# Performance work log

Measured on AMD Instinct MI355X. Metric: run time of the kernel, lower is better.

Reference implementation:

```python
import jax, jax.numpy as jnp
import numpy as np

NEG_INF = -1.0e9
LN_EPS = 1e-5
LEAK = 0.2


def setup_inputs() -> dict:
    key = jax.random.key(0)
    ks = jax.random.split(key, 8)
    B, C, T, N, H = 8, 64, 24, 512, 2
    hd = C // H
    x = jax.random.normal(ks[0], (B, C, T, N), dtype=jnp.float32)
    gso = jax.random.randint(ks[1], (N, N), 0, 2, dtype=jnp.int32)
    # torch nn.Linear weights are (out, in); xavier-ish scale
    s = (2.0 / (C + C)) ** 0.5
    Wq = jax.random.normal(ks[2], (C, C), dtype=jnp.float32) * s
    Wk = jax.random.normal(ks[3], (C, C), dtype=jnp.float32) * s
    Wv = jax.random.normal(ks[4], (C, C), dtype=jnp.float32) * s
    sa = (2.0 / (H + hd)) ** 0.5
    a_src = jax.random.normal(ks[5], (H, hd), dtype=jnp.float32) * sa
    a_dst = jax.random.normal(ks[6], (H, hd), dtype=jnp.float32) * sa
    ln_gamma = jnp.ones((C,), dtype=jnp.float32)
    ln_beta = jnp.zeros((C,), dtype=jnp.float32)
    return {"x": x, "gso": gso, "Wq": Wq, "Wk": Wk, "Wv": Wv,
            "a_src": a_src, "a_dst": a_dst, "ln_gamma": ln_gamma, "ln_beta": ln_beta}


def _spatial_gat(x, gso, Wq, Wk, Wv, a_src, a_dst, ln_gamma, ln_beta):
    B, C, T, N = x.shape
    H, hd = a_src.shape
    # (B, C, T, N) -> (B*T, N, C)
    xr = jnp.transpose(x, (0, 2, 3, 1)).reshape(B * T, N, C)
    # torch Linear: y = x @ W.T
    Q = jnp.einsum('bnc,dc->bnd', xr, Wq).reshape(B * T, N, H, hd)
    K = jnp.einsum('bnc,dc->bnd', xr, Wk).reshape(B * T, N, H, hd)
    V = jnp.einsum('bnc,dc->bnd', xr, Wv).reshape(B * T, N, H, hd)
    # additive GAT scores, all heads at once
    s_src = jnp.einsum('bnhd,hd->bnh', Q, a_src)  # (BT, N, H)
    s_dst = jnp.einsum('bnhd,hd->bnh', K, a_dst)  # (BT, N, H)
    scores = jax.nn.leaky_relu(s_src[:, :, None, :] + s_dst[:, None, :, :], LEAK)  # (BT, Ni, Nj, H)
    mask = jnp.where(gso == 0, jnp.float32(NEG_INF), jnp.float32(0.0))  # (N, N)
    scores = scores + mask[None, :, :, None]
    attn = jax.nn.softmax(scores, axis=2)  # softmax over destination j
    out = jnp.einsum('bijh,bjhd->bihd', attn, V)  # (BT, N, H, hd)
    out = out.reshape(B * T, N, C)
    # LayerNorm over channel dim
    mu = jnp.mean(out, axis=-1, keepdims=True)
    var = jnp.var(out, axis=-1, keepdims=True)
    out = (out - mu) * jax.lax.rsqrt(var + LN_EPS) * ln_gamma + ln_beta
    # back to (B, C, T, N)
    return jnp.transpose(out.reshape(B, T, N, C), (0, 3, 1, 2))


def reference(x, gso, Wq, Wk, Wv, a_src, a_dst, ln_gamma, ln_beta):
    return _spatial_gat(x, gso, Wq, Wk, Wv, a_src, a_dst, ln_gamma, ln_beta)
```

## Files before the change

### kernel.cpp

```cpp
#include <hip/hip_runtime.h>

#define CDIM 64
#define TDIM 24
#define NDIM 512
#define NBT  192

typedef float    float4v __attribute__((ext_vector_type(4)));
typedef _Float16 half8v  __attribute__((ext_vector_type(8)));
typedef _Float16 half4v  __attribute__((ext_vector_type(4)));
typedef _Float16 half2v  __attribute__((ext_vector_type(2)));


__device__ __forceinline__ float exp2_fast(float x) {
#if __has_builtin(__builtin_amdgcn_exp2f)
  return __builtin_amdgcn_exp2f(x);
#else
  return __expf(x * 0.69314718f);
#endif
}

struct SmemK1 {
  union {
    _Float16 xt[128][72];
    _Float16 vtb[64][136];
  } big;
  _Float16 wv[64][72];
  _Float16 wext[16][72];
};

__launch_bounds__(256, 2)
__global__ void k1_v(const float* __restrict__ x,  const float* __restrict__ Wv,
                     const float* __restrict__ Wq, const float* __restrict__ Wk,
                     const float* __restrict__ a_src, const float* __restrict__ a_dst,
                     const int* __restrict__ gso,
                     _Float16* __restrict__ VT_g,
                     float* __restrict__ s_src_g, float* __restrict__ s_dst_g,
                     unsigned char* __restrict__ maskb) {
  const int t  = threadIdx.x;
  const int bx = blockIdx.x;

  if (bx >= 768) {
    int g = (bx - 768) * 256 + t;
    const int4* gp = (const int4*)gso + (size_t)g * 4;
    unsigned w[4];
#pragma unroll
    for (int k = 0; k < 4; ++k) {
      int4 v = gp[k];
      w[k] = (v.x ? 0x000000FFu : 0u) | (v.y ? 0x0000FF00u : 0u) |
             (v.z ? 0x00FF0000u : 0u) | (v.w ? 0xFF000000u : 0u);
    }
    uint4 o; o.x = w[0]; o.y = w[1]; o.z = w[2]; o.w = w[3];
    ((uint4*)maskb)[g] = o;
    return;
  }

  __shared__ SmemK1 sm;
  const int qn = bx & 3;
  const int bt = bx >> 2;
  const int b  = bt / TDIM, tt = bt % TDIM;
  const int n0 = qn * 128;

#pragma unroll
  for (int it = 0; it < 4; ++it) {
    int idx = it * 256 + t;
    float4 vv = ((const float4*)Wv)[idx];
    int d = idx >> 4, k4 = (idx & 15) * 4;
    half4v h4; h4[0] = (_Float16)vv.x; h4[1] = (_Float16)vv.y;
    h4[2] = (_Float16)vv.z; h4[3] = (_Float16)vv.w;
    *(half4v*)&sm.wv[d][k4] = h4;
  }
  for (int z = t; z < 12 * 72; z += 256) ((_Float16*)sm.wext[4])[z] = (_Float16)0.f;
  if (t < 64) {
    int c = t;
    float s0 = 0.f, s1 = 0.f, d0 = 0.f, d1 = 0.f;
#pragma unroll
    for (int d = 0; d < 32; ++d) {
      s0 += a_src[d]      * Wq[d * 64 + c];
      s1 += a_src[32 + d] * Wq[(32 + d) * 64 + c];
      d0 += a_dst[d]      * Wk[d * 64 + c];
      d1 += a_dst[32 + d] * Wk[(32 + d) * 64 + c];
    }
    const float l2e = 1.44269504f;
    sm.wext[0][c] = (_Float16)(s0 * l2e); sm.wext[1][c] = (_Float16)(s1 * l2e);
    sm.wext[2][c] = (_Float16)(d0 * l2e); sm.wext[3][c] = (_Float16)(d1 * l2e);
  }
  for (int it = 0; it < 16; ++it) {
    int idx = it * 256 + t;
    int cp = idx >> 7, n = idx & 127;
    int c0 = cp * 2;
    const float* base = x + ((size_t)(b * CDIM + c0) * TDIM + tt) * NDIM + n0 + n;
    half2v p; p[0] = (_Float16)base[0]; p[1] = (_Float16)base[(size_t)TDIM * NDIM];
    *(half2v*)&sm.big.xt[n][c0] = p;
  }
  __syncthreads();

  const int lane = t & 63, w = t >> 6;
  const int m = lane & 15, quad = lane >> 4;
  const int mbase = w * 32;

  float4v acc[2][5];
#pragma unroll
  for (int mt = 0; mt < 2; ++mt)
#pragma unroll
    for (int nt = 0; nt < 5; ++nt)
#pragma unroll
      for (int r = 0; r < 4; ++r) acc[mt][nt][r] = 0.f;

#pragma unroll
  for (int ks = 0; ks < 2; ++ks) {
    half8v af[2], bf[5];
#pragma unroll
    for (int mt = 0; mt < 2; ++mt)
      af[mt] = *(const half8v*)&sm.big.xt[mbase + mt * 16 + m][ks * 32 + quad * 8];
#pragma unroll
    for (int nt = 0; nt < 4; ++nt)
      bf[nt] = *(const half8v*)&sm.wv[nt * 16 + m][ks * 32 + quad * 8];
    bf[4] = *(const half8v*)&sm.wext[m][ks * 32 + quad * 8];
#pragma unroll
    for (int mt = 0; mt < 2; ++mt)
#pragma unroll
      for (int nt = 0; nt < 5; ++nt)
        acc[mt][nt] = __builtin_amdgcn_mfma_f32_16x16x32_f16(af[mt], bf[nt], acc[mt][nt], 0, 0, 0);
  }

  if (m < 4) {
    float* basep = (m < 2 ? s_src_g : s_dst_g) + (size_t)(bt * 2 + (m & 1)) * NDIM;
#pragma unroll
    for (int mt = 0; mt < 2; ++mt)
#pragma unroll
      for (int r = 0; r < 4; ++r)
        basep[n0 + mbase + mt * 16 + quad * 4 + r] = acc[mt][4][r];
  }
  __syncthreads();

#pragma unroll
  for (int mt = 0; mt < 2; ++mt)
#pragma unroll
    for (int nt = 0; nt < 4; ++nt)
#pragma unroll
      for (int r = 0; r < 4; r += 2) {
        int nl = mbase + mt * 16 + quad * 4 + r;
        int c  = nt * 16 + m;
        half2v p = __builtin_bit_cast(half2v,
            __builtin_amdgcn_cvt_pkrtz(acc[mt][nt][r], acc[mt][nt][r + 1]));
        *(half2v*)&sm.big.vtb[c][nl] = p;
      }
  __syncthreads();

  const uint4* vq = (const uint4*)sm.big.vtb;
#pragma unroll
  for (int it = 0; it < 4; ++it) {
    int idx = it * 256 + t;
    int c = idx >> 4, q4 = idx & 15;
    ((uint4*)VT_g)[(size_t)(bt * 64 + c) * 64 + qn * 16 + q4] = vq[c * 17 + q4];
  }
}

struct SmemK2 {
  union {
    struct { _Float16 vt[64][128]; } s;
    struct { float otile[64][66]; float rsum[4][64]; float rsq[4][64];
             float mu[64]; float rs[64]; } e;
  } u;
  _Float16 sF16[2][512];
  _Float16 sP16[2][512];
};

__launch_bounds__(256, 4)
__global__ void k2_attn(const _Float16* __restrict__ VT_g,
                        const float* __restrict__ s_src_g, const float* __restrict__ s_dst_g,
                        const unsigned char* __restrict__ maskb,
                        const float* __restrict__ gamma, const float* __restrict__ beta,
                        float* __restrict__ out) {
  __shared__ SmemK2 sm;
  const int t     = threadIdx.x;
  const int id    = blockIdx.x;
  const int itile = (id >> 3) & 7;
  const int bt    = ((id >> 6) << 3) | (id & 7);
  const int i0    = itile * 64;
  const int b     = bt / TDIM, tt = bt % TDIM;
  const int lane  = t & 63, w = t >> 6;
  const int h = w >> 1, ihalf = w & 1;
  const int m = lane & 15, quad = lane >> 4;

  for (int it = 0; it < 4; ++it) {
    int idx = it * 256 + t;
    float d = s_dst_g[(size_t)bt * 2 * NDIM + idx];
    ((_Float16*)sm.sF16)[idx] = (_Float16)exp2_fast(d);
    ((_Float16*)sm.sP16)[idx] = (_Float16)exp2_fast(0.2f * d);
  }
  half8v E8[2], Q8[2];
#pragma unroll
  for (int mt = 0; mt < 2; ++mt) {
    float sv = s_src_g[(size_t)(bt * 2 + h) * NDIM + i0 + ihalf * 32 + mt * 16 + m];
    _Float16 ev = (_Float16)exp2_fast(sv - 6.f);
    _Float16 qv = (_Float16)exp2_fast(0.2f * sv - 6.f);
#pragma unroll
    for (int jj = 0; jj < 8; ++jj) { E8[mt][jj] = ev; Q8[mt][jj] = qv; }
  }

  float4v acc[2][2], accs[2];
#pragma unroll
  for (int mt = 0; mt < 2; ++mt) {
#pragma unroll
    for (int r = 0; r < 4; ++r) { acc[mt][0][r] = 0.f; acc[mt][1][r] = 0.f; accs[mt][r] = 0.f; }
  }
  const half8v bones = {(_Float16)1.f, (_Float16)1.f, (_Float16)1.f, (_Float16)1.f,
                        (_Float16)1.f, (_Float16)1.f, (_Float16)1.f, (_Float16)1.f};

  const uint4* vsrc = (const uint4*)VT_g;
  uint4 pv0, pv1, pv2, pv3;
  const int vc  = t >> 4;
  const int vch = t & 15;
  const int vswz = (vch * 8) ^ ((vc & 7) * 8);

  const unsigned char* mb0 = maskb + (size_t)(i0 + ihalf * 32 + m) * NDIM + quad * 8;
  const unsigned char* mb1 = mb0 + (size_t)16 * NDIM;

#define PREFETCH(js_)                                                          \
  {                                                                            \
    pv0 = vsrc[(size_t)(bt * 64 + vc     ) * 64 + (js_) * 16 + vch];           \
    pv1 = vsrc[(size_t)(bt * 64 + vc + 16) * 64 + (js_) * 16 + vch];           \
    pv2 = vsrc[(size_t)(bt * 64 + vc + 32) * 64 + (js_) * 16 + vch];           \
    pv3 = vsrc[(size_t)(bt * 64 + vc + 48) * 64 + (js_) * 16 + vch];           \
  }

  PREFETCH(0);

#pragma unroll
  for (int js = 0; js < 4; ++js) {
    __syncthreads();
    *(uint4*)&sm.u.s.vt[vc     ][vswz] = pv0;
    *(uint4*)&sm.u.s.vt[vc + 16][vswz] = pv1;
    *(uint4*)&sm.u.s.vt[vc + 32][vswz] = pv2;
    *(uint4*)&sm.u.s.vt[vc + 48][vswz] = pv3;
    __syncthreads();
    if (js < 3) PREFETCH(js + 1);

    uint2 mk[2][4];
#pragma unroll
    for (int mt = 0; mt < 2; ++mt) {
      const unsigned char* mbp = (mt ? mb1 : mb0) + js * 128;
#pragma unroll
      for (int ksl = 0; ksl < 4; ++ksl)
        mk[mt][ksl] = *(const uint2*)(mbp + ksl * 32);
    }

#pragma unroll
    for (int ksl = 0; ksl < 4; ++ksl) {
      int jq = ksl * 32 + quad * 8;
      half8v F8 = *(const half8v*)&sm.sF16[h][js * 128 + jq];
      half8v P8 = *(const half8v*)&sm.sP16[h][js * 128 + jq];
      int vbase = (h * 32 + m) * 128 + (jq ^ ((m & 7) * 8));
      half8v b0 = *(const half8v*)&sm.u.s.vt[0][vbase];
      half8v b1 = *(const half8v*)&sm.u.s.vt[0][vbase + 16 * 128];
#pragma unroll
      for (int mt = 0; mt < 2; ++mt) {
        unsigned mw0 = mk[mt][ksl].x, mw1 = mk[mt][ksl].y;
        half8v e8 = __builtin_elementwise_max(E8[mt] * F8, Q8[mt] * P8);
        uint4 eu = __builtin_bit_cast(uint4, e8);
        eu.x &= __builtin_amdgcn_perm(0u, mw0, 0x01010000u);
        eu.y &= __builtin_amdgcn_perm(0u, mw0, 0x03030202u);
        eu.z &= __builtin_amdgcn_perm(0u, mw1, 0x01010000u);
        eu.w &= __builtin_amdgcn_perm(0u, mw1, 0x03030202u);
        half8v af = __builtin_bit_cast(half8v, eu);
        acc[mt][0] = __builtin_amdgcn_mfma_f32_16x16x32_f16(af, b0,    acc[mt][0], 0, 0, 0);
        acc[mt][1] = __builtin_amdgcn_mfma_f32_16x16x32_f16(af, b1,    acc[mt][1], 0, 0, 0);
        accs[mt]   = __builtin_amdgcn_mfma_f32_16x16x32_f16(af, bones, accs[mt],   0, 0, 0);
      }
    }
  }
#undef PREFETCH

  __syncthreads();
#pragma unroll
  for (int mt = 0; mt < 2; ++mt)
#pragma unroll
    for (int r = 0; r < 4; ++r) {
      float sc = __builtin_amdgcn_rcpf(accs[mt][r]);
      int i_loc = ihalf * 32 + mt * 16 + quad * 4 + r;
#pragma unroll
      for (int nt = 0; nt < 2; ++nt)
        sm.u.e.otile[i_loc][h * 32 + nt * 16 + m] = acc[mt][nt][r] * sc;
    }
  __syncthreads();

  {
    int i = t & 63, cg = t >> 6;
    float s1 = 0.f, s2 = 0.f;
#pragma unroll
    for (int cc = 0; cc < 16; ++cc) {
      float v = sm.u.e.otile[i][cg * 16 + cc];
      s1 += v; s2 += v * v;
    }
    sm.u.e.rsum[cg][i] = s1;
    sm.u.e.rsq[cg][i]  = s2;
  }
  __syncthreads();
  if (t < 64) {
    int i = t;
    float s1 = 0.f, s2 = 0.f;
#pragma unroll
    for (int cg = 0; cg < 4; ++cg) { s1 += sm.u.e.rsum[cg][i]; s2 += sm.u.e.rsq[cg][i]; }
    float mu  = s1 * (1.f / 64.f);
    float var = s2 * (1.f / 64.f) - mu * mu;
    sm.u.e.mu[i] = mu;
    sm.u.e.rs[i] = rsqrtf(var + 1e-5f);
  }
  __syncthreads();
  {
    int i = t & 63, cg = t >> 6;
    float mu = sm.u.e.mu[i], rs = sm.u.e.rs[i];
    int n = i0 + i;
#pragma unroll
    for (int cc = 0; cc < 16; ++cc) {
      int c = cg * 16 + cc;
      float v = (sm.u.e.otile[i][c] - mu) * rs * gamma[c] + beta[c];
      out[((size_t)(b * CDIM + c) * TDIM + tt) * NDIM + n] = v;
    }
  }
}

extern "C" void kernel_launch(void* const* d_in, const int* in_sizes, int n_in,
                              void* d_out, int out_size, void* d_ws, size_t ws_size,
                              hipStream_t stream) {
  const float* x     = (const float*)d_in[0];
  const int*   gso   = (const int*)d_in[1];
  const float* Wq    = (const float*)d_in[2];
  const float* Wk    = (const float*)d_in[3];
  const float* Wv    = (const float*)d_in[4];
  const float* a_src = (const float*)d_in[5];
  const float* a_dst = (const float*)d_in[6];
  const float* gamma = (const float*)d_in[7];
  const float* beta  = (const float*)d_in[8];
  float* out = (float*)d_out;

  char* ws = (char*)d_ws;
  _Float16* VT_g  = (_Float16*)ws;
  float*    s_src = (float*)(ws + 12582912);
  float*    s_dst = (float*)(ws + 13369344);
  unsigned char* maskb = (unsigned char*)(ws + 14155776);

  k1_v<<<832, 256, 0, stream>>>(x, Wv, Wq, Wk, a_src, a_dst, gso,
                                VT_g, s_src, s_dst, maskb);
  k2_attn<<<1536, 256, 0, stream>>>(VT_g, s_src, s_dst, maskb, gamma, beta, out);
}
```

Measured before the change: 127.4 us.

## Double k2 attention row tile to 128 rows to reuse staged V per block

The attention kernel now processes 128 query rows per block instead of 64, halving the grid to 768 blocks. Each block's staged V tile and destination-score vectors serve twice as many rows, which halves the global V traffic and the LDS staging and sync cost per row. The per-row exponent math is rewritten on packed half2 values to save registers, and launch bounds change (k2 to 3 waves/SIMD, k1 to 4). The cost is more accumulator registers per thread, a larger LDS epilogue tile and fewer blocks to fill the device.

```diff
diff --git a/kernel.cpp b/kernel.cpp
--- a/kernel.cpp
+++ b/kernel.cpp
@@ -28,7 +28,7 @@
   _Float16 wext[16][72];
 };
 
-__launch_bounds__(256, 2)
+__launch_bounds__(256, 4)
 __global__ void k1_v(const float* __restrict__ x,  const float* __restrict__ Wv,
                      const float* __restrict__ Wq, const float* __restrict__ Wk,
                      const float* __restrict__ a_src, const float* __restrict__ a_dst,
@@ -159,14 +159,14 @@
 struct SmemK2 {
   union {
     struct { _Float16 vt[64][128]; } s;
-    struct { float otile[64][66]; float rsum[4][64]; float rsq[4][64];
-             float mu[64]; float rs[64]; } e;
+    struct { float otile[128][66]; float rsum[2][128]; float rsq[2][128];
+             float mu[128]; float rs[128]; } e;
   } u;
   _Float16 sF16[2][512];
   _Float16 sP16[2][512];
 };
 
-__launch_bounds__(256, 4)
+__launch_bounds__(256, 3)
 __global__ void k2_attn(const _Float16* __restrict__ VT_g,
                         const float* __restrict__ s_src_g, const float* __restrict__ s_dst_g,
                         const unsigned char* __restrict__ maskb,
@@ -175,13 +175,14 @@
   __shared__ SmemK2 sm;
   const int t     = threadIdx.x;
   const int id    = blockIdx.x;
-  const int itile = (id >> 3) & 7;
-  const int bt    = ((id >> 6) << 3) | (id & 7);
-  const int i0    = itile * 64;
+  const int itile = (id >> 3) & 3;
+  const int bt    = ((id >> 5) << 3) | (id & 7);
+  const int i0    = itile * 128;
   const int b     = bt / TDIM, tt = bt % TDIM;
   const int lane  = t & 63, w = t >> 6;
   const int h = w >> 1, ihalf = w & 1;
   const int m = lane & 15, quad = lane >> 4;
+  const int rbase = ihalf * 64;
 
   for (int it = 0; it < 4; ++it) {
     int idx = it * 256 + t;
@@ -189,22 +190,21 @@
     ((_Float16*)sm.sF16)[idx] = (_Float16)exp2_fast(d);
     ((_Float16*)sm.sP16)[idx] = (_Float16)exp2_fast(0.2f * d);
   }
-  half8v E8[2], Q8[2];
-#pragma unroll
-  for (int mt = 0; mt < 2; ++mt) {
-    float sv = s_src_g[(size_t)(bt * 2 + h) * NDIM + i0 + ihalf * 32 + mt * 16 + m];
+  half2v e2[4], q2[4];
+#pragma unroll
+  for (int mt = 0; mt < 4; ++mt) {
+    float sv = s_src_g[(size_t)(bt * 2 + h) * NDIM + i0 + rbase + mt * 16 + m];
     _Float16 ev = (_Float16)exp2_fast(sv - 6.f);
     _Float16 qv = (_Float16)exp2_fast(0.2f * sv - 6.f);
-#pragma unroll
-    for (int jj = 0; jj < 8; ++jj) { E8[mt][jj] = ev; Q8[mt][jj] = qv; }
-  }
-
-  float4v acc[2][2], accs[2];
-#pragma unroll
-  for (int mt = 0; mt < 2; ++mt) {
+    e2[mt][0] = ev; e2[mt][1] = ev;
+    q2[mt][0] = qv; q2[mt][1] = qv;
+  }
+
+  float4v acc[4][2], accs[4];
+#pragma unroll
+  for (int mt = 0; mt < 4; ++mt)
 #pragma unroll
     for (int r = 0; r < 4; ++r) { acc[mt][0][r] = 0.f; acc[mt][1][r] = 0.f; accs[mt][r] = 0.f; }
-  }
   const half8v bones = {(_Float16)1.f, (_Float16)1.f, (_Float16)1.f, (_Float16)1.f,
                         (_Float16)1.f, (_Float16)1.f, (_Float16)1.f, (_Float16)1.f};
 
@@ -214,8 +214,7 @@
   const int vch = t & 15;
   const int vswz = (vch * 8) ^ ((vc & 7) * 8);
 
-  const unsigned char* mb0 = maskb + (size_t)(i0 + ihalf * 32 + m) * NDIM + quad * 8;
-  const unsigned char* mb1 = mb0 + (size_t)16 * NDIM;
+  const unsigned char* mrow = maskb + (size_t)(i0 + rbase + m) * NDIM + quad * 8;
 
 #define PREFETCH(js_)                                                          \
   {                                                                            \
@@ -237,10 +236,10 @@
     __syncthreads();
     if (js < 3) PREFETCH(js + 1);
 
-    uint2 mk[2][4];
-#pragma unroll
-    for (int mt = 0; mt < 2; ++mt) {
-      const unsigned char* mbp = (mt ? mb1 : mb0) + js * 128;
+    uint2 mk[4][4];
+#pragma unroll
+    for (int mt = 0; mt < 4; ++mt) {
+      const unsigned char* mbp = mrow + (size_t)(mt * 16) * NDIM + js * 128;
 #pragma unroll
       for (int ksl = 0; ksl < 4; ++ksl)
         mk[mt][ksl] = *(const uint2*)(mbp + ksl * 32);
@@ -254,15 +253,28 @@
       int vbase = (h * 32 + m) * 128 + (jq ^ ((m & 7) * 8));
       half8v b0 = *(const half8v*)&sm.u.s.vt[0][vbase];
       half8v b1 = *(const half8v*)&sm.u.s.vt[0][vbase + 16 * 128];
-#pragma unroll
-      for (int mt = 0; mt < 2; ++mt) {
+      uint4 fu = __builtin_bit_cast(uint4, F8);
+      uint4 pu = __builtin_bit_cast(uint4, P8);
+      half2v f2a = __builtin_bit_cast(half2v, fu.x), f2b = __builtin_bit_cast(half2v, fu.y);
+      half2v f2c = __builtin_bit_cast(half2v, fu.z), f2d = __builtin_bit_cast(half2v, fu.w);
+      half2v p2a = __builtin_bit_cast(half2v, pu.x), p2b = __builtin_bit_cast(half2v, pu.y);
+      half2v p2c = __builtin_bit_cast(half2v, pu.z), p2d = __builtin_bit_cast(half2v, pu.w);
+#pragma unroll
+      for (int mt = 0; mt < 4; ++mt) {
         unsigned mw0 = mk[mt][ksl].x, mw1 = mk[mt][ksl].y;
-        half8v e8 = __builtin_elementwise_max(E8[mt] * F8, Q8[mt] * P8);
-        uint4 eu = __builtin_bit_cast(uint4, e8);
-        eu.x &= __builtin_amdgcn_perm(0u, mw0, 0x01010000u);
-        eu.y &= __builtin_amdgcn_perm(0u, mw0, 0x03030202u);
-        eu.z &= __builtin_amdgcn_perm(0u, mw1, 0x01010000u);
-        eu.w &= __builtin_amdgcn_perm(0u, mw1, 0x03030202u);
+        uint4 eu;
+        eu.x = __builtin_bit_cast(unsigned,
+                 __builtin_elementwise_max(e2[mt] * f2a, q2[mt] * p2a)) &
+               __builtin_amdgcn_perm(0u, mw0, 0x01010000u);
+        eu.y = __builtin_bit_cast(unsigned,
+                 __builtin_elementwise_max(e2[mt] * f2b, q2[mt] * p2b)) &
+               __builtin_amdgcn_perm(0u, mw0, 0x03030202u);
+        eu.z = __builtin_bit_cast(unsigned,
+                 __builtin_elementwise_max(e2[mt] * f2c, q2[mt] * p2c)) &
+               __builtin_amdgcn_perm(0u, mw1, 0x01010000u);
+        eu.w = __builtin_bit_cast(unsigned,
+                 __builtin_elementwise_max(e2[mt] * f2d, q2[mt] * p2d)) &
+               __builtin_amdgcn_perm(0u, mw1, 0x03030202u);
         half8v af = __builtin_bit_cast(half8v, eu);
         acc[mt][0] = __builtin_amdgcn_mfma_f32_16x16x32_f16(af, b0,    acc[mt][0], 0, 0, 0);
         acc[mt][1] = __builtin_amdgcn_mfma_f32_16x16x32_f16(af, b1,    acc[mt][1], 0, 0, 0);
@@ -274,11 +286,11 @@
 
   __syncthreads();
 #pragma unroll
-  for (int mt = 0; mt < 2; ++mt)
+  for (int mt = 0; mt < 4; ++mt)
 #pragma unroll
     for (int r = 0; r < 4; ++r) {
       float sc = __builtin_amdgcn_rcpf(accs[mt][r]);
-      int i_loc = ihalf * 32 + mt * 16 + quad * 4 + r;
+      int i_loc = rbase + mt * 16 + quad * 4 + r;
 #pragma unroll
       for (int nt = 0; nt < 2; ++nt)
         sm.u.e.otile[i_loc][h * 32 + nt * 16 + m] = acc[mt][nt][r] * sc;
@@ -286,22 +298,21 @@
   __syncthreads();
 
   {
-    int i = t & 63, cg = t >> 6;
+    int i = t & 127, cg = t >> 7;
     float s1 = 0.f, s2 = 0.f;
 #pragma unroll
-    for (int cc = 0; cc < 16; ++cc) {
-      float v = sm.u.e.otile[i][cg * 16 + cc];
+    for (int cc = 0; cc < 32; ++cc) {
+      float v = sm.u.e.otile[i][cg * 32 + cc];
       s1 += v; s2 += v * v;
     }
     sm.u.e.rsum[cg][i] = s1;
     sm.u.e.rsq[cg][i]  = s2;
   }
   __syncthreads();
-  if (t < 64) {
+  if (t < 128) {
     int i = t;
-    float s1 = 0.f, s2 = 0.f;
-#pragma unroll
-    for (int cg = 0; cg < 4; ++cg) { s1 += sm.u.e.rsum[cg][i]; s2 += sm.u.e.rsq[cg][i]; }
+    float s1 = sm.u.e.rsum[0][i] + sm.u.e.rsum[1][i];
+    float s2 = sm.u.e.rsq[0][i]  + sm.u.e.rsq[1][i];
     float mu  = s1 * (1.f / 64.f);
     float var = s2 * (1.f / 64.f) - mu * mu;
     sm.u.e.mu[i] = mu;
@@ -309,12 +320,12 @@
   }
   __syncthreads();
   {
-    int i = t & 63, cg = t >> 6;
+    int i = t & 127, cg = t >> 7;
     float mu = sm.u.e.mu[i], rs = sm.u.e.rs[i];
     int n = i0 + i;
 #pragma unroll
-    for (int cc = 0; cc < 16; ++cc) {
-      int c = cg * 16 + cc;
+    for (int cc = 0; cc < 32; ++cc) {
+      int c = cg * 32 + cc;
       float v = (sm.u.e.otile[i][c] - mu) * rs * gamma[c] + beta[c];
       out[((size_t)(b * CDIM + c) * TDIM + tt) * NDIM + n] = v;
     }
@@ -343,5 +354,5 @@
 
   k1_v<<<832, 256, 0, stream>>>(x, Wv, Wq, Wk, a_src, a_dst, gso,
                                 VT_g, s_src, s_dst, maskb);
-  k2_attn<<<1536, 256, 0, stream>>>(VT_g, s_src, s_dst, maskb, gamma, beta, out);
+  k2_attn<<<768, 256, 0, stream>>>(VT_g, s_src, s_dst, maskb, gamma, beta, out);
 }
```

Result: faster. 121.7 us (median of 2 runs) (-4.4%).
